# Kernel tuning notes

Hardware: AMD Instinct MI355X
Metric: run time of the kernel (lower is better)

Reference implementation:

```python
import jax, jax.numpy as jnp
import numpy as np
import math

B, H, N, D = 4, 8, 2048, 64


def setup_inputs() -> dict:
    key = jax.random.key(0)
    kq, kk, kv = jax.random.split(key, 3)
    q = jax.random.normal(kq, (B, H, N, D), dtype=jnp.float32)
    k = jax.random.normal(kk, (B, H, N, D), dtype=jnp.float32)
    v = jax.random.normal(kv, (B, H, N, D), dtype=jnp.float32)
    return {"q": q, "k": k, "v": v}


def reference(q, k, v):
    # global_attention_Sub: expanded squared L2 distance ||q_i - k_j||^2
    # = qq_i - 2 q_i.k_j + kk_j, then softmax(-dist/sqrt(D)) @ v.
    scale = math.sqrt(q.shape[-1])
    inner = -2.0 * jnp.einsum('bhnd,bhmd->bhnm', q, k)          # [B,H,N,N]
    qq = jnp.sum(q * q, axis=-1, keepdims=True)                  # [B,H,N,1]
    kk = jnp.sum(k * k, axis=-1, keepdims=True)                  # [B,H,N,1]
    diff_sq = qq + inner + jnp.swapaxes(kk, -1, -2)              # [B,H,N,N]
    attn = jax.nn.softmax(-diff_sq / scale, axis=-1)
    x = jnp.einsum('bhnm,bhmd->bhnd', attn, v)                   # [B,H,N,D]
    return jnp.transpose(x, (0, 2, 1, 3))                        # [B,N,H,D]
```

## Files before the change

kernel.cpp:

```cpp
#include <hip/hip_runtime.h>

typedef __bf16 bf16x8 __attribute__((ext_vector_type(8)));
typedef float floatx4 __attribute__((ext_vector_type(4)));
typedef float floatx16 __attribute__((ext_vector_type(16)));
typedef unsigned int uintx4 __attribute__((ext_vector_type(4)));

constexpr int Bc = 4, Hc = 8, Nc = 2048, Dc = 64;
constexpr int BQ = 128;
constexpr int WQ = 32;
constexpr int TK = 64;
constexpr int NT = Nc / TK;
constexpr int NT2 = NT / 2;
constexpr float LOG2E = 1.44269504088896340736f;

constexpr size_t KSW_OFF = 0;
constexpr size_t VSW_OFF = (size_t)32 * NT * 8192;
constexpr size_t KKN_OFF = VSW_OFF * 2;

constexpr int SK_OFF = 0;
constexpr int SV_OFF = 32768;
constexpr int SL_OFF = 65536;
constexpr int SMEM_BYTES = 65536 + 1024;

typedef __attribute__((address_space(1))) const unsigned int gu32;
typedef __attribute__((address_space(3))) unsigned int lu32;
__device__ __forceinline__ void dma16(const void* g, void* l) {
    __builtin_amdgcn_global_load_lds((gu32*)g, (lu32*)l, 16, 0, 0);
}

__device__ __forceinline__ unsigned pk2(float lo, float hi) {
    unsigned short a = __builtin_bit_cast(unsigned short, (__bf16)lo);
    unsigned short b = __builtin_bit_cast(unsigned short, (__bf16)hi);
    return (unsigned)a | ((unsigned)b << 16);
}

__global__ __launch_bounds__(256) void prep_kernel(
    const float* __restrict__ Kg, const float* __restrict__ Vg, char* __restrict__ ws)
{
    __shared__ float sT[64 * 68];
    const int tid = threadIdx.x;
    const int jt = blockIdx.x, bh = blockIdx.y;

    __bf16* Ksw = (__bf16*)(ws + KSW_OFF) + ((size_t)bh * NT + jt) * 4096;
    __bf16* Vsw = (__bf16*)(ws + VSW_OFF) + ((size_t)bh * NT + jt) * 4096;
    float*  kkn = (float*)(ws + KKN_OFF) + (size_t)bh * Nc + jt * 64;
    const size_t tb = ((size_t)bh * Nc + jt * 64) * Dc;

#pragma unroll
    for (int cc = 0; cc < 2; ++cc) {
        const int g   = tid + cc * 256;
        const int key = g >> 3, kcx = g & 7;
        const int kc  = kcx ^ (key & 7);
        const float* src = Kg + tb + key * 64 + kc * 8;
        float4 a = *(const float4*)src;
        float4 b = *(const float4*)(src + 4);
        float ss = a.x*a.x + a.y*a.y + a.z*a.z + a.w*a.w
                 + b.x*b.x + b.y*b.y + b.z*b.z + b.w*b.w;
        ss += __shfl_xor(ss, 1);
        ss += __shfl_xor(ss, 2);
        ss += __shfl_xor(ss, 4);
        if (kcx == 0) {
            const int k5 = key & 31, kt = key >> 5;
            const int rlo = k5 & 3, hh = (k5 >> 2) & 1, rhi = k5 >> 3;
            kkn[kt * 32 + hh * 16 + rhi * 4 + rlo] = -(ss * 0.125f * LOG2E);
        }
        bf16x8 c8;
        c8[0]=(__bf16)a.x; c8[1]=(__bf16)a.y; c8[2]=(__bf16)a.z; c8[3]=(__bf16)a.w;
        c8[4]=(__bf16)b.x; c8[5]=(__bf16)b.y; c8[6]=(__bf16)b.z; c8[7]=(__bf16)b.w;
        *(bf16x8*)(Ksw + g * 8) = c8;
    }
    {
        const int js = tid >> 2, dc = (tid & 3) * 16;
        const float* vr = Vg + tb + js * 64 + dc;
        float* dst = &sT[js * 68 + dc];
        *(float4*)dst       = *(const float4*)vr;
        *(float4*)(dst + 4) = *(const float4*)(vr + 4);
        *(float4*)(dst + 8) = *(const float4*)(vr + 8);
        *(float4*)(dst + 12)= *(const float4*)(vr + 12);
    }
    __syncthreads();
#pragma unroll
    for (int cc = 0; cc < 2; ++cc) {
        const int g = tid + cc * 256;
        const int d = g >> 3, kcx = g & 7;
        const int kc = kcx ^ (d & 7);
        bf16x8 c8;
#pragma unroll
        for (int e = 0; e < 8; ++e) {
            const int ee = (e + kcx) & 7;
            c8[ee] = (__bf16)sT[(kc * 8 + ee) * 68 + d];
        }
        *(bf16x8*)(Vsw + g * 8) = c8;
    }
}

__global__ __launch_bounds__(512, 4) void attn_kernel(
    const float* __restrict__ Qg, const char* __restrict__ ws, float* __restrict__ Og)
{
    __shared__ __align__(16) char smem[SMEM_BYTES];

    const int tid  = threadIdx.x;
    const int wave = tid >> 6;
    const int grp  = wave >> 2;
    const int sw   = wave & 3;
    const int lane = tid & 63;
    const int r31  = lane & 31;
    const int hi   = lane >> 5;

    const int lin  = blockIdx.x + (blockIdx.y << 4);
    const int xcd  = lin & 7, slot = lin >> 3;
    const int bh   = (xcd << 2) | (slot >> 4);
    const int qt   = slot & 15;

    const char* Kimg = ws + KSW_OFF + (size_t)bh * NT * 8192;
    const char* Vimg = ws + VSW_OFF + (size_t)bh * NT * 8192;
    const float* kkp = (const float*)(ws + KKN_OFF) + (size_t)bh * Nc;

    const float qscale = 0.25f * LOG2E;
    const int i0 = qt * BQ + sw * WQ;

    bf16x8 qf[4];
    {
        const float* qrow = Qg + ((size_t)bh * Nc + i0 + r31) * Dc + hi * 8;
#pragma unroll
        for (int ks = 0; ks < 4; ++ks) {
            float4 a = *(const float4*)(qrow + ks * 16);
            float4 b = *(const float4*)(qrow + ks * 16 + 4);
            bf16x8 f;
            f[0] = (__bf16)(a.x * qscale); f[1] = (__bf16)(a.y * qscale);
            f[2] = (__bf16)(a.z * qscale); f[3] = (__bf16)(a.w * qscale);
            f[4] = (__bf16)(b.x * qscale); f[5] = (__bf16)(b.y * qscale);
            f[6] = (__bf16)(b.z * qscale); f[7] = (__bf16)(b.w * qscale);
            qf[ks] = f;
        }
    }

    int off4[4];
#pragma unroll
    for (int ks = 0; ks < 4; ++ks)
        off4[ks] = r31 * 128 + (((ks * 2 + hi) ^ (r31 & 7)) << 4);

    floatx16 oacc[2];
#pragma unroll
    for (int dt = 0; dt < 2; ++dt)
#pragma unroll
        for (int e = 0; e < 16; ++e) oacc[dt][e] = 0.f;
    float lpr = 0.f;

    floatx16 zacc;
#pragma unroll
    for (int e = 0; e < 16; ++e) zacc[e] = 0.f;

    auto stage = [&](int t, int nb) {
        const size_t tb = (size_t)t * 16384;
        const int off = tid * 16;
        dma16(Kimg + tb + off,        smem + SK_OFF + nb * 8192 + off);
        dma16(Kimg + tb + 8192 + off, smem + SK_OFF + 16384 + nb * 8192 + off);
        dma16(Vimg + tb + off,        smem + SV_OFF + nb * 8192 + off);
        dma16(Vimg + tb + 8192 + off, smem + SV_OFF + 16384 + nb * 8192 + off);
    };

    stage(0, 0);

    for (int t = 0; t < NT2; ++t) {
        const int b = t & 1;
        __syncthreads();
        if (t + 1 < NT2) stage(t + 1, b ^ 1);

        const int jt = 2 * t + grp;
        const char* kb = smem + SK_OFF + grp * 16384 + b * 8192;
        const char* vb = smem + SV_OFF + grp * 16384 + b * 8192;

        floatx16 kkv[2];
        const float* kkb = kkp + jt * 64 + hi * 16;
#pragma unroll
        for (int kt = 0; kt < 2; ++kt)
#pragma unroll
            for (int gi = 0; gi < 4; ++gi) {
                floatx4 kv = *(const floatx4*)(kkb + kt * 32 + gi * 4);
                kkv[kt][gi * 4 + 0] = kv[0]; kkv[kt][gi * 4 + 1] = kv[1];
                kkv[kt][gi * 4 + 2] = kv[2]; kkv[kt][gi * 4 + 3] = kv[3];
            }

        floatx16 st[2];
        __builtin_amdgcn_s_setprio(1);
#pragma unroll
        for (int kt = 0; kt < 2; ++kt) {
            bf16x8 kf0 = *(const bf16x8*)(kb + kt * 4096 + off4[0]);
            st[kt] = __builtin_amdgcn_mfma_f32_32x32x16_bf16(kf0, qf[0], zacc, 0, 0, 0);
#pragma unroll
            for (int ks = 1; ks < 4; ++ks) {
                bf16x8 kf = *(const bf16x8*)(kb + kt * 4096 + off4[ks]);
                st[kt] = __builtin_amdgcn_mfma_f32_32x32x16_bf16(kf, qf[ks], st[kt], 0, 0, 0);
            }
        }
        __builtin_amdgcn_s_setprio(0);

#pragma unroll
        for (int kt = 0; kt < 2; ++kt) {
            float p[16];
#pragma unroll
            for (int r = 0; r < 16; ++r) {
                p[r] = __builtin_amdgcn_exp2f(st[kt][r] + kkv[kt][r]);
                lpr += p[r];
            }
            unsigned w[4][2];
#pragma unroll
            for (int g = 0; g < 4; ++g) {
                w[g][0] = pk2(p[4 * g + 0], p[4 * g + 1]);
                w[g][1] = pk2(p[4 * g + 2], p[4 * g + 3]);
            }
            __builtin_amdgcn_s_setprio(1);
#pragma unroll
            for (int sub = 0; sub < 2; ++sub) {
                unsigned a0 = w[2 * sub][0],     a1 = w[2 * sub][1];
                unsigned b0 = w[2 * sub + 1][0], b1 = w[2 * sub + 1][1];
                asm("v_permlane32_swap_b32 %0, %1" : "+v"(a0), "+v"(b0));
                asm("v_permlane32_swap_b32 %0, %1" : "+v"(a1), "+v"(b1));
                uintx4 u; u[0] = a0; u[1] = a1; u[2] = b0; u[3] = b1;
                bf16x8 pa = __builtin_bit_cast(bf16x8, u);
                const int ks = kt * 2 + sub;
#pragma unroll
                for (int dt = 0; dt < 2; ++dt) {
                    bf16x8 vf = *(const bf16x8*)(vb + dt * 4096 + off4[ks]);
                    oacc[dt] = __builtin_amdgcn_mfma_f32_32x32x16_bf16(pa, vf, oacc[dt], 0, 0, 0);
                }
            }
            __builtin_amdgcn_s_setprio(0);
        }
    }

    {
        float l = lpr + __shfl_xor(lpr, 32);
        if (!hi) *(float*)(smem + SL_OFF + (grp * 128 + sw * 32 + r31) * 4) = l;
    }
    __syncthreads();

    {
        char* slot = smem + wave * 4096;
        if (grp == 0) {
#pragma unroll
            for (int r = 0; r < 16; ++r)
                *(float*)(slot + r * 256 + lane * 4) = oacc[1][r];
        } else {
#pragma unroll
            for (int r = 0; r < 16; ++r)
                *(float*)(slot + r * 256 + lane * 4) = oacc[0][r];
        }
    }
    __syncthreads();

    floatx16 osum;
    if (grp == 0) osum = oacc[0]; else osum = oacc[1];
    {
        const char* pslot = smem + (wave ^ 4) * 4096;
#pragma unroll
        for (int r = 0; r < 16; ++r)
            osum[r] += *(const float*)(pslot + r * 256 + lane * 4);
    }

    const float* slp = (const float*)(smem + SL_OFF);
    const int b_ = bh >> 3, hh = bh & 7;
#pragma unroll
    for (int g = 0; g < 4; ++g) {
        floatx4 la = *(const floatx4*)(slp + sw * 32 + 8 * g + 4 * hi);
        floatx4 lb = *(const floatx4*)(slp + 128 + sw * 32 + 8 * g + 4 * hi);
#pragma unroll
        for (int rlo = 0; rlo < 4; ++rlo) {
            const float inv = 1.f / (la[rlo] + lb[rlo]);
            const int i = i0 + 8 * g + 4 * hi + rlo;
            float* orow = Og + (((size_t)b_ * Nc + i) * Hc + hh) * Dc + grp * 32 + r31;
            orow[0] = osum[4 * g + rlo] * inv;
        }
    }
}

extern "C" void kernel_launch(void* const* d_in, const int* in_sizes, int n_in,
                              void* d_out, int out_size, void* d_ws, size_t ws_size,
                              hipStream_t stream) {
    const float* q = (const float*)d_in[0];
    const float* k = (const float*)d_in[1];
    const float* v = (const float*)d_in[2];
    float* out = (float*)d_out;
    char* ws = (char*)d_ws;
    prep_kernel<<<dim3(NT, Bc * Hc), 256, 0, stream>>>(k, v, ws);
    attn_kernel<<<dim3(Nc / BQ, Bc * Hc), 512, 0, stream>>>(q, ws, out);
}
```

Measured before the change: 149.6 us.

## Stage key norms in LDS via DMA and seed MFMA accumulator with them

Key squared-norm bias values are now copied into shared memory alongside the K/V tiles with async global-to-LDS loads, instead of each thread reading them from global memory every iteration. The QK^T MFMA accumulator is initialized with these bias values, so the per-element add before exp2 disappears. The row-sum accumulation is also split into two independent chains to shorten the dependency chain. This adds a small LDS buffer and a few extra DMA instructions per stage, and it relies on the existing barrier to order the norm copy.

Result: faster. 136.0 us (-9.1%).

```diff
diff --git a/kernel.cpp b/kernel.cpp
--- a/kernel.cpp
+++ b/kernel.cpp
@@ -17,15 +17,19 @@
 constexpr size_t VSW_OFF = (size_t)32 * NT * 8192;
 constexpr size_t KKN_OFF = VSW_OFF * 2;
 
-constexpr int SK_OFF = 0;
-constexpr int SV_OFF = 32768;
-constexpr int SL_OFF = 65536;
-constexpr int SMEM_BYTES = 65536 + 1024;
+constexpr int SK_OFF  = 0;
+constexpr int SV_OFF  = 32768;
+constexpr int SKK_OFF = 65536;
+constexpr int SL_OFF  = 66560;
+constexpr int SMEM_BYTES = 67584;
 
 typedef __attribute__((address_space(1))) const unsigned int gu32;
 typedef __attribute__((address_space(3))) unsigned int lu32;
 __device__ __forceinline__ void dma16(const void* g, void* l) {
     __builtin_amdgcn_global_load_lds((gu32*)g, (lu32*)l, 16, 0, 0);
+}
+__device__ __forceinline__ void dma4(const void* g, void* l) {
+    __builtin_amdgcn_global_load_lds((gu32*)g, (lu32*)l, 4, 0, 0);
 }
 
 __device__ __forceinline__ unsigned pk2(float lo, float hi) {
@@ -145,11 +149,7 @@
     for (int dt = 0; dt < 2; ++dt)
 #pragma unroll
         for (int e = 0; e < 16; ++e) oacc[dt][e] = 0.f;
-    float lpr = 0.f;
-
-    floatx16 zacc;
-#pragma unroll
-    for (int e = 0; e < 16; ++e) zacc[e] = 0.f;
+    float lpr0 = 0.f, lpr1 = 0.f;
 
     auto stage = [&](int t, int nb) {
         const size_t tb = (size_t)t * 16384;
@@ -158,6 +158,8 @@
         dma16(Kimg + tb + 8192 + off, smem + SK_OFF + 16384 + nb * 8192 + off);
         dma16(Vimg + tb + off,        smem + SV_OFF + nb * 8192 + off);
         dma16(Vimg + tb + 8192 + off, smem + SV_OFF + 16384 + nb * 8192 + off);
+        if (tid < 128)
+            dma4(kkp + t * 128 + tid, smem + SKK_OFF + nb * 512 + tid * 4);
     };
 
     stage(0, 0);
@@ -167,43 +169,37 @@
         __syncthreads();
         if (t + 1 < NT2) stage(t + 1, b ^ 1);
 
-        const int jt = 2 * t + grp;
         const char* kb = smem + SK_OFF + grp * 16384 + b * 8192;
         const char* vb = smem + SV_OFF + grp * 16384 + b * 8192;
-
-        floatx16 kkv[2];
-        const float* kkb = kkp + jt * 64 + hi * 16;
+        const float* skkb = (const float*)(smem + SKK_OFF + b * 512) + grp * 64 + hi * 16;
+
+        floatx16 st[2];
 #pragma unroll
         for (int kt = 0; kt < 2; ++kt)
 #pragma unroll
             for (int gi = 0; gi < 4; ++gi) {
-                floatx4 kv = *(const floatx4*)(kkb + kt * 32 + gi * 4);
-                kkv[kt][gi * 4 + 0] = kv[0]; kkv[kt][gi * 4 + 1] = kv[1];
-                kkv[kt][gi * 4 + 2] = kv[2]; kkv[kt][gi * 4 + 3] = kv[3];
-            }
-
-        floatx16 st[2];
+                floatx4 kv = *(const floatx4*)(skkb + kt * 32 + gi * 4);
+                st[kt][gi * 4 + 0] = kv[0]; st[kt][gi * 4 + 1] = kv[1];
+                st[kt][gi * 4 + 2] = kv[2]; st[kt][gi * 4 + 3] = kv[3];
+            }
+
         __builtin_amdgcn_s_setprio(1);
 #pragma unroll
-        for (int kt = 0; kt < 2; ++kt) {
-            bf16x8 kf0 = *(const bf16x8*)(kb + kt * 4096 + off4[0]);
-            st[kt] = __builtin_amdgcn_mfma_f32_32x32x16_bf16(kf0, qf[0], zacc, 0, 0, 0);
-#pragma unroll
-            for (int ks = 1; ks < 4; ++ks) {
+        for (int kt = 0; kt < 2; ++kt)
+#pragma unroll
+            for (int ks = 0; ks < 4; ++ks) {
                 bf16x8 kf = *(const bf16x8*)(kb + kt * 4096 + off4[ks]);
                 st[kt] = __builtin_amdgcn_mfma_f32_32x32x16_bf16(kf, qf[ks], st[kt], 0, 0, 0);
             }
-        }
         __builtin_amdgcn_s_setprio(0);
 
 #pragma unroll
         for (int kt = 0; kt < 2; ++kt) {
             float p[16];
 #pragma unroll
-            for (int r = 0; r < 16; ++r) {
-                p[r] = __builtin_amdgcn_exp2f(st[kt][r] + kkv[kt][r]);
-                lpr += p[r];
-            }
+            for (int r = 0; r < 16; ++r) p[r] = __builtin_amdgcn_exp2f(st[kt][r]);
+#pragma unroll
+            for (int r = 0; r < 16; r += 2) { lpr0 += p[r]; lpr1 += p[r + 1]; }
             unsigned w[4][2];
 #pragma unroll
             for (int g = 0; g < 4; ++g) {
@@ -231,6 +227,7 @@
     }
 
     {
+        float lpr = lpr0 + lpr1;
         float l = lpr + __shfl_xor(lpr, 32);
         if (!hi) *(float*)(smem + SL_OFF + (grp * 128 + sw * 32 + r31) * 4) = l;
     }
```
